# Kernel tuning notes

Measured on AMD Instinct MI355X. Metric: run time of the kernel, lower is better.

The kernel has to match this reference:

```python
import jax, jax.numpy as jnp
import numpy as np

N = 32768       # nodes
E = 65536       # directed edges
B = 512         # graphs (N // B = 64 atoms each)
DIM = 64
NUM_FEAT = 14
EDGE_DIM = 4
NET_HID = 128
CONV_STEPS = 12
S2S_STEPS = 3
NSTEM = 1024
NUM_OUT_STEM = 105

leaky = lambda v: jax.nn.leaky_relu(v, 0.01)


def setup_inputs():
    key = jax.random.key(0)
    ks = jax.random.split(key, 30)
    p = lambda i, shape, s=0.1: jax.random.normal(ks[i], shape, jnp.float32) * s
    return {
        'x': jax.random.normal(ks[0], (N, NUM_FEAT), jnp.float32),
        'edge_attr': jax.random.uniform(ks[1], (E, EDGE_DIM), jnp.float32),
        'edge_index': jax.random.randint(ks[2], (2, E), 0, N),
        'batch': jnp.arange(N, dtype=jnp.int32) // (N // B),  # sorted graph ids, all graphs non-empty
        'stem_idx': jax.random.randint(ks[3], (NSTEM,), 0, N),
        'lin0_w': p(4, (DIM, NUM_FEAT)), 'lin0_b': p(5, (DIM,)),
        'net_w1': p(6, (NET_HID, EDGE_DIM)), 'net_b1': p(7, (NET_HID,)),
        'net_w2': p(8, (DIM * DIM, NET_HID), 0.05), 'net_b2': p(9, (DIM * DIM,), 0.05),
        'conv_root': p(10, (DIM, DIM)), 'conv_bias': p(11, (DIM,)),
        'gru_w_ih': p(12, (3 * DIM, DIM)), 'gru_w_hh': p(13, (3 * DIM, DIM)),
        'gru_b_ih': p(14, (3 * DIM,)), 'gru_b_hh': p(15, (3 * DIM,)),
        'lin1_w': p(16, (8 * DIM, DIM)), 'lin1_b': p(17, (8 * DIM,)),
        'lin2_w': p(18, (NUM_OUT_STEM, 8 * DIM)), 'lin2_b': p(19, (NUM_OUT_STEM,)),
        's2s_w_ih': p(20, (4 * DIM, 2 * DIM)), 's2s_w_hh': p(21, (4 * DIM, DIM)),
        's2s_b_ih': p(22, (4 * DIM,)), 's2s_b_hh': p(23, (4 * DIM,)),
        'lin3_w': p(24, (1, 2 * DIM)), 'lin3_b': p(25, (1,)),
    }


def reference(x, edge_attr, edge_index, batch, stem_idx,
              lin0_w, lin0_b, net_w1, net_b1, net_w2, net_b2,
              conv_root, conv_bias, gru_w_ih, gru_w_hh, gru_b_ih, gru_b_hh,
              lin1_w, lin1_b, lin2_w, lin2_b,
              s2s_w_ih, s2s_w_hh, s2s_b_ih, s2s_b_hh, lin3_w, lin3_b):
    src, dst = edge_index[0], edge_index[1]

    out = leaky(x @ lin0_w.T + lin0_b)               # [N, DIM]
    h = out

    # edge-conditioned weights: constant across conv steps (edge_attr fixed), hoist
    W = (leaky(edge_attr @ net_w1.T + net_b1) @ net_w2.T + net_b2).reshape(E, DIM, DIM)

    deg = jax.ops.segment_sum(jnp.ones((E,), jnp.float32), dst, num_segments=N)
    inv_deg = (1.0 / jnp.maximum(deg, 1.0))[:, None]

    def step(carry, _):
        out, h = carry
        # NNConv: gather src feats, per-edge matmul, scatter-mean to dst, plus root term
        msg = jnp.einsum('ei,eio->eo', out[src], W)                           # [E, DIM]
        agg = jax.ops.segment_sum(msg, dst, num_segments=N) * inv_deg        # scatter-mean
        m = leaky(agg + out @ conv_root + conv_bias)
        # GRU cell (torch gate order r, z, n)
        gi = m @ gru_w_ih.T + gru_b_ih
        gh = h @ gru_w_hh.T + gru_b_hh
        ir, iz, i_n = jnp.split(gi, 3, axis=-1)
        hr, hz, hn = jnp.split(gh, 3, axis=-1)
        r = jax.nn.sigmoid(ir + hr)
        z = jax.nn.sigmoid(iz + hz)
        n = jnp.tanh(i_n + r * hn)
        h_new = (1.0 - z) * n + z * h
        return (h_new, h_new), None

    (out, h), _ = jax.lax.scan(step, (out, h), None, length=CONV_STEPS)

    # per-stem head (stem_idx = precomputed flat node indices)
    stem_feat = out[stem_idx]                                                # [NSTEM, DIM]
    per_stem_out = leaky(stem_feat @ lin1_w.T + lin1_b) @ lin2_w.T + lin2_b  # [NSTEM, 105]

    # Set2Set readout (LSTM with torch gate order i, f, g, o)
    q_star = jnp.zeros((B, 2 * DIM), jnp.float32)
    hh = jnp.zeros((B, DIM), jnp.float32)
    cc = jnp.zeros((B, DIM), jnp.float32)
    for _ in range(S2S_STEPS):
        gates = q_star @ s2s_w_ih.T + s2s_b_ih + hh @ s2s_w_hh.T + s2s_b_hh
        gi_, gf_, gg_, go_ = jnp.split(gates, 4, axis=-1)
        cc = jax.nn.sigmoid(gf_) * cc + jax.nn.sigmoid(gi_) * jnp.tanh(gg_)
        hh = jax.nn.sigmoid(go_) * jnp.tanh(cc)
        q = hh                                                               # [B, DIM]
        e = jnp.sum(out * q[batch], axis=-1)                                 # [N]
        emax = jax.ops.segment_max(e, batch, num_segments=B)
        ee = jnp.exp(e - emax[batch])
        a = ee / jax.ops.segment_sum(ee, batch, num_segments=B)[batch]       # segment softmax
        r_read = jax.ops.segment_sum(a[:, None] * out, batch, num_segments=B)
        q_star = jnp.concatenate([q, r_read], axis=-1)

    sout = q_star @ lin3_w.T + lin3_b                                        # [B, 1]
    return sout, per_stem_out


if __name__ == '__main__':
    o = reference(**setup_inputs())
    print(o[0].shape, o[1].shape)
```

## Files before the change

### kernel.cpp

```cpp
#include <hip/hip_runtime.h>
#include <hip/hip_bf16.h>

#define N_NODES   32768
#define N_EDGES   65536
#define NGRAPH    512
#define DIM       64
#define NFEAT     14
#define NHID      128
#define WCOLS     4096
#define NSTEM     1024
#define NOUT      105

typedef __attribute__((ext_vector_type(8))) short short8;
typedef __attribute__((ext_vector_type(4))) float f32x4;

__device__ __forceinline__ float bf2f(unsigned int u16) {
  union { unsigned int i; float f; } c; c.i = u16 << 16; return c.f;
}
__device__ __forceinline__ unsigned short f2bf(float f) {
  union { float f; unsigned int i; } c; c.f = f;
  return (unsigned short)((c.i + 0x7fffu + ((c.i >> 16) & 1u)) >> 16);
}
__device__ __forceinline__ float leaky(float x) { return x > 0.f ? x : 0.01f * x; }
__device__ __forceinline__ float sigm(float x) { return 1.f / (1.f + expf(-x)); }
// ... 2 lines not shown

constexpr size_t OFF_HIDP = 0;
constexpr size_t SZ_HIDP  = (size_t)N_EDGES * NHID * 2;
constexpr size_t OFF_T2T  = ALN(OFF_HIDP + SZ_HIDP);
constexpr size_t SZ_T2T   = (size_t)WCOLS * NHID * 2;
constexpr size_t OFF_B2T  = ALN(OFF_T2T + SZ_T2T);
constexpr size_t SZ_B2T   = (size_t)WCOLS * 4;
constexpr size_t OFF_STATE= ALN(OFF_B2T + SZ_B2T);
constexpr size_t SZ_STATE = (size_t)N_NODES * DIM * 4;
constexpr size_t OFF_AGG  = ALN(OFF_STATE + SZ_STATE);
constexpr size_t SZ_AGG   = SZ_STATE;
constexpr size_t OFF_IDEG = ALN(OFF_AGG + SZ_AGG);
constexpr size_t SZ_IDEG  = (size_t)N_NODES * 4;
constexpr size_t OFF_CNT  = ALN(OFF_IDEG + SZ_IDEG);
constexpr size_t SZ_CNT   = (size_t)N_NODES * 4;
constexpr size_t OFF_RP   = ALN(OFF_CNT + SZ_CNT);
constexpr size_t SZ_RP    = (size_t)(N_NODES + 1) * 4;
constexpr size_t OFF_CUR  = ALN(OFF_RP + SZ_RP);
constexpr size_t SZ_CUR   = (size_t)N_NODES * 4;
constexpr size_t OFF_SRCP = ALN(OFF_CUR + SZ_CUR);
constexpr size_t SZ_SRCP  = (size_t)N_EDGES * 4;
constexpr size_t OFF_DSTP = ALN(OFF_SRCP + SZ_SRCP);
constexpr size_t SZ_DSTP  = (size_t)N_EDGES * 4;
constexpr size_t OFF_EPOS = ALN(OFF_DSTP + SZ_DSTP);
constexpr size_t SZ_EPOS  = (size_t)N_EDGES * 4;
constexpr size_t OFF_BW1  = ALN(OFF_EPOS + SZ_EPOS);
constexpr size_t SZ_BW1   = 256 * 64 * 2;
constexpr size_t OFF_BW2  = ALN(OFF_BW1 + SZ_BW1);
constexpr size_t SZ_BW2   = 192 * 64 * 2;
constexpr size_t OFF_WIH  = ALN(OFF_BW2 + SZ_BW2);
constexpr size_t SZ_WIH   = 128 * 256 * 4;
constexpr size_t OFF_WHH  = ALN(OFF_WIH + SZ_WIH);
constexpr size_t SZ_WHH   = 64 * 256 * 4;
constexpr size_t OFF_SCL  = ALN(OFF_WHH + SZ_WHH);
constexpr size_t SZ_SCL   = (size_t)N_EDGES * 64 * 4;
constexpr size_t OFF_WT   = ALN(OFF_SCL + SZ_SCL);

__global__ void k_deg(const int* __restrict__ dst, int* __restrict__ cnt) {
  int e = blockIdx.x * 256 + threadIdx.x;
  atomicAdd(&cnt[dst[e]], 1);
}
__global__ __launch_bounds__(1024) void k_scan(const int* __restrict__ cnt,
                                               int* __restrict__ rp,
                                               int* __restrict__ cur,
                                               float* __restrict__ ideg) {
  __shared__ int part[1024];
  const int t = threadIdx.x, base = t * 32;
  int s = 0;
  for (int i = 0; i < 32; ++i) s += cnt[base + i];
  part[t] = s;
  __syncthreads();
  for (int off = 1; off < 1024; off <<= 1) {
    int v = (t >= off) ? part[t - off] : 0;
    __syncthreads();
    part[t] += v;
    __syncthreads();
  }
  int run = part[t] - s;
  for (int i = 0; i < 32; ++i) {
    int c = cnt[base + i];
    rp[base + i] = run; cur[base + i] = run;
    ideg[base + i] = 1.0f / fmaxf((float)c, 1.0f);
    run += c;
  }
  if (t == 1023) rp[N_NODES] = run;
}
__global__ void k_permute(const int* __restrict__ src, const int* __restrict__ dst,
// ... 16 lines not shown
                           const float* __restrict__ wih,
                           unsigned short* __restrict__ BW1, unsigned short* __restrict__ BW2) {
  int gid = blockIdx.x * 256 + threadIdx.x;
  if (gid >= 64 * 448) return;
  int i = gid / 448, c = gid % 448;
  if (c < 64)        BW1[c * 64 + i] = f2bf(root[i * 64 + c]);
  else if (c < 256)  BW1[c * 64 + i] = f2bf(whh[(c - 64) * 64 + i]);
  else               BW2[(c - 256) * 64 + i] = f2bf(wih[(c - 256) * 64 + i]);
}
__global__ void k_prep_s2s(const float* __restrict__ wih, const float* __restrict__ whh,
                           float* __restrict__ wihT, float* __restrict__ whhT) {
  int gid = blockIdx.x * 256 + threadIdx.x;
  if (gid < 32768) { int j = gid >> 8, k = gid & 255; wihT[gid] = wih[k * 128 + j]; }
  else { int g2 = gid - 32768; int j = g2 >> 8, k = g2 & 255; whhT[g2] = whh[k * 64 + j]; }
}
__global__ void k_lin0(const float* __restrict__ x, const float* __restrict__ w,
                       const float* __restrict__ b, float* __restrict__ state) {
  int gid = blockIdx.x * 256 + threadIdx.x;
  int n = gid >> 6, o = gid & 63;
  float acc = b[o];
  #pragma unroll
  for (int f = 0; f < NFEAT; ++f) acc += x[(size_t)n * NFEAT + f] * w[o * NFEAT + f];
  state[gid] = leaky(acc);
}
__global__ void k_hidden(const float* __restrict__ ea, const float* __restrict__ w1,
                         const float* __restrict__ b1, const int* __restrict__ epos,
                         unsigned short* __restrict__ hid_p) {
  int gid = blockIdx.x * 256 + threadIdx.x;
  int e = gid >> 7, h = gid & 127;
  float acc = b1[h];
  #pragma unroll
  for (int d = 0; d < 4; ++d) acc += ea[(size_t)e * 4 + d] * w1[h * 4 + d];
  hid_p[(size_t)epos[e] * 128 + h] = f2bf(leaky(acc));
}

#define WG_PAD 136
__global__ __launch_bounds__(256) void k_wgemm(const unsigned short* __restrict__ A,
                                               const unsigned short* __restrict__ Bt,
                                               const float* __restrict__ b2t,
                                               unsigned char* __restrict__ W8,
                                               float* __restrict__ SCL) {
  __shared__ __align__(16) unsigned short As[64 * WG_PAD];
  __shared__ __align__(16) unsigned short Bs[64 * WG_PAD];
  __shared__ __align__(16) char pk[64][64];
  const int nb = blockIdx.x, mb = blockIdx.y, t = threadIdx.x;
  #pragma unroll
  for (int j = 0; j < 4; ++j) {
    int c = t + 256 * j;
    int row = c >> 4, col8 = (c & 15) * 8;
    *reinterpret_cast<uint4*>(&As[row * WG_PAD + col8]) =
        *reinterpret_cast<const uint4*>(A + (size_t)(mb * 64 + row) * 128 + col8);
    *reinterpret_cast<uint4*>(&Bs[row * WG_PAD + col8]) =
        *reinterpret_cast<const uint4*>(Bt + (size_t)(nb * 64 + row) * 128 + col8);
  }
  __syncthreads();
  const int wv = t >> 6, ln = t & 63, r = ln & 15, g = ln >> 4;
  f32x4 acc[4] = {};
  #pragma unroll
  for (int ks = 0; ks < 4; ++ks) {
    int k0 = ks * 32 + g * 8;
    short8 a = *reinterpret_cast<const short8*>(&As[(wv * 16 + r) * WG_PAD + k0]);
    #pragma unroll
    for (int nt = 0; nt < 4; ++nt) {
      short8 b = *reinterpret_cast<const short8*>(&Bs[(nt * 16 + r) * WG_PAD + k0]);
      acc[nt] = __builtin_amdgcn_mfma_f32_16x16x32_bf16(a, b, acc[nt], 0, 0, 0);
    }
  }
  float bias[4];
  #pragma unroll
  for (int nt = 0; nt < 4; ++nt) bias[nt] = b2t[nb * 64 + nt * 16 + r];
  #pragma unroll
  for (int j = 0; j < 4; ++j) {
    int e_l = wv * 16 + g * 4 + j;
    float w[4], m = 0.f;
    #pragma unroll
    for (int nt = 0; nt < 4; ++nt) { w[nt] = acc[nt][j] + bias[nt]; m = fmaxf(m, fabsf(w[nt])); }
    m = fmaxf(m, __shfl_xor(m, 1)); m = fmaxf(m, __shfl_xor(m, 2));
    m = fmaxf(m, __shfl_xor(m, 4)); m = fmaxf(m, __shfl_xor(m, 8));
    float inv = m > 0.f ? 127.f / m : 0.f;
    #pragma unroll
    for (int nt = 0; nt < 4; ++nt)
      pk[e_l][nt * 16 + r] = (char)(int)rintf(w[nt] * inv);
    if (r == 0) {
      size_t e8 = (size_t)mb * 64 + e_l;
      SCL[e8 * 64 + nb] = m * (1.f / 127.f);
    }
  }
  __syncthreads();
  {
    int e_l = t >> 2, jc = t & 3;
    size_t e8 = (size_t)mb * 64 + e_l;
    *reinterpret_cast<uint4*>(W8 + e8 * 4096 + jc * 1024 + nb * 16) =
        *reinterpret_cast<const uint4*>(&pk[e_l][jc * 16]);
  }
}

__global__ __launch_bounds__(256) void k_msg_csr(const unsigned char* __restrict__ W8,
                                                 const float* __restrict__ SCL,
                                                 int lim8,
                                                 const int* __restrict__ rp,
                                                 const int* __restrict__ src_p,
                                                 const float* __restrict__ state,
                                                 const float* __restrict__ ideg,
                                                 float* __restrict__ agg) {
  const int wv = threadIdx.x >> 6, ln = threadIdx.x & 63;
  const int d = blockIdx.x * 4 + wv;
  const int k0 = rp[d], k1 = rp[d + 1];
  float acc = 0.f;
  for (int k = k0; k < k1; ++k) {
    if (k >= lim8) continue;
    const int src = src_p[k];
    const float sval = state[(size_t)src * 64 + ln];
    const unsigned char* wp = W8 + (size_t)k * 4096 + ln * 16;
    float sub = 0.f;
    #pragma unroll
    for (int j = 0; j < 4; ++j) {
      uint4 v = *reinterpret_cast<const uint4*>(wp + j * 1024);
      unsigned int u[4] = {v.x, v.y, v.z, v.w};
      #pragma unroll
      for (int q = 0; q < 4; ++q) {
        int i0 = j * 16 + q * 4;
        sub = fmaf((float)(int)(char)(u[q] & 0xff),         __shfl(sval, i0),     sub);
        sub = fmaf((float)(int)(char)((u[q] >> 8) & 0xff),  __shfl(sval, i0 + 1), sub);
        sub = fmaf((float)(int)(char)((u[q] >> 16) & 0xff), __shfl(sval, i0 + 2), sub);
        sub = fmaf((float)(int)(char)(u[q] >> 24),          __shfl(sval, i0 + 3), sub);
      }
    }
    acc = fmaf(sub, SCL[(size_t)k * 64 + ln], acc);
  }
  agg[(size_t)d * 64 + ln] = acc * ideg[d];
}

#define WM_PAD 136
__global__ __launch_bounds__(256) void k_wmsg(const unsigned short* __restrict__ hid,
                                              const unsigned short* __restrict__ T2t,
                                              const float* __restrict__ b2t,
                                              const float* __restrict__ state,
                                              const int* __restrict__ srcs,
                                              const int* __restrict__ dsts,
                                              const float* __restrict__ ideg,
                                              int e0,
                                              float* __restrict__ agg) {
  __shared__ __align__(16) unsigned short As[64 * WM_PAD];
  __shared__ __align__(16) unsigned short Bs[2][64 * WM_PAD];
  __shared__ __align__(16) float Ss[64][68];
  __shared__ int dstl[64]; __shared__ float idgl[64];
  __shared__ int srcl[64];
  const int t = threadIdx.x;
  const int eb = blockIdx.x * 64;
  if (t < 64) {
    int e = e0 + eb + t;
    srcl[t] = srcs[e];
    int d = dsts[e]; dstl[t] = d; idgl[t] = ideg[d];
  }
  __syncthreads();
  #pragma unroll
  for (int j = 0; j < 4; ++j) {
    int c = t + 256 * j;
    int row = c >> 4, col8 = (c & 15) * 8;
    *reinterpret_cast<uint4*>(&As[row * WM_PAD + col8]) =
        *reinterpret_cast<const uint4*>(hid + (size_t)(eb + row) * 128 + col8);
  }
  #pragma unroll
  for (int j = 0; j < 4; ++j) {
    int c = t + 256 * j;
    int row = c >> 4, q = (c & 15) * 4;
    *reinterpret_cast<float4*>(&Ss[row][q]) =
        *reinterpret_cast<const float4*>(state + (size_t)srcl[row] * 64 + q);
  }
  #pragma unroll
  for (int j = 0; j < 4; ++j) {
    int c = t + 256 * j;
    int row = c >> 4, col8 = (c & 15) * 8;
    *reinterpret_cast<uint4*>(&Bs[0][row * WM_PAD + col8]) =
        *reinterpret_cast<const uint4*>(T2t + (size_t)row * 128 + col8);
  }
  __syncthreads();
  const int wv = t >> 6, ln = t & 63, r = ln & 15, g = ln >> 4;
  for (int nb = 0; nb < 64; ++nb) {
    const int cur = nb & 1;
    if (nb + 1 < 64) {
      #pragma unroll
      for (int j = 0; j < 4; ++j) {
        int c = t + 256 * j;
        int row = c >> 4, col8 = (c & 15) * 8;
        *reinterpret_cast<uint4*>(&Bs[cur ^ 1][row * WM_PAD + col8]) =
            *reinterpret_cast<const uint4*>(T2t + (size_t)((nb + 1) * 64 + row) * 128 + col8);
      }
    }
    f32x4 acc[4] = {};
    #pragma unroll
    for (int ks = 0; ks < 4; ++ks) {
      int k0 = ks * 32 + g * 8;
      short8 a = *reinterpret_cast<const short8*>(&As[(wv * 16 + r) * WM_PAD + k0]);
      #pragma unroll
      for (int nt = 0; nt < 4; ++nt) {
        short8 b = *reinterpret_cast<const short8*>(&Bs[cur][(nt * 16 + r) * WM_PAD + k0]);
        acc[nt] = __builtin_amdgcn_mfma_f32_16x16x32_bf16(a, b, acc[nt], 0, 0, 0);
      }
    }
    float bias[4];
    #pragma unroll
    for (int nt = 0; nt < 4; ++nt) bias[nt] = b2t[nb * 64 + nt * 16 + r];
    float pj[4];
    #pragma unroll
    for (int j = 0; j < 4; ++j) {
      int row = wv * 16 + g * 4 + j;
      float p = 0.f;
      #pragma unroll
      for (int nt = 0; nt < 4; ++nt)
        p += (acc[nt][j] + bias[nt]) * Ss[row][nt * 16 + r];
      pj[j] = p;
    }
    #pragma unroll
    for (int j = 0; j < 4; ++j) {
      float p = pj[j];
      p += __shfl_xor(p, 1); p += __shfl_xor(p, 2);
      p += __shfl_xor(p, 4); p += __shfl_xor(p, 8);
      pj[j] = p;
    }
    if (r == 0) {
      #pragma unroll
      for (int j = 0; j < 4; ++j) {
        int row = wv * 16 + g * 4 + j;
        atomicAdd(&agg[(size_t)dstl[row] * 64 + nb], pj[j] * idgl[row]);
      }
    }
    __syncthreads();
  }
}

#define KPAD 72
__global__ __launch_bounds__(512, 1) void k_gru(const float* __restrict__ agg,
                                                float* __restrict__ state,
                                                const unsigned short* __restrict__ BW1,
                                                const unsigned short* __restrict__ BW2,
                                                const float* __restrict__ conv_bias,
                                                const float* __restrict__ b_ih,
                                                const float* __restrict__ b_hh) {
  __shared__ __align__(16) unsigned short As[128 * KPAD];
  __shared__ __align__(16) unsigned short Ms[128 * KPAD];
  __shared__ __align__(16) unsigned short B1s[256 * KPAD];
  __shared__ __align__(16) unsigned short B2s[192 * KPAD];
  const int t = threadIdx.x;
  const int rowbase = blockIdx.x * 128;
  #pragma unroll
  for (int j = 0; j < 2; ++j) {
    int c = t + 512 * j;
    int row = c >> 3, col8 = (c & 7) * 8;
    const float* sp = state + (size_t)(rowbase + row) * 64 + col8;
    float4 f0 = *reinterpret_cast<const float4*>(sp);
    float4 f1 = *reinterpret_cast<const float4*>(sp + 4);
    short8 hv;
    hv[0] = (short)f2bf(f0.x); hv[1] = (short)f2bf(f0.y);
    hv[2] = (short)f2bf(f0.z); hv[3] = (short)f2bf(f0.w);
    hv[4] = (short)f2bf(f1.x); hv[5] = (short)f2bf(f1.y);
    hv[6] = (short)f2bf(f1.z); hv[7] = (short)f2bf(f1.w);
    *reinterpret_cast<short8*>(&As[row * KPAD + col8]) = hv;
  }
  #pragma unroll
  for (int j = 0; j < 4; ++j) {
    int c = t + 512 * j;
    int row = c >> 3, col8 = (c & 7) * 8;
    *reinterpret_cast<uint4*>(&B1s[row * KPAD + col8]) =
        *reinterpret_cast<const uint4*>(BW1 + row * 64 + col8);
  }
  #pragma unroll
  for (int j = 0; j < 3; ++j) {
    int c = t + 512 * j;
    int row = c >> 3, col8 = (c & 7) * 8;
    *reinterpret_cast<uint4*>(&B2s[row * KPAD + col8]) =
        *reinterpret_cast<const uint4*>(BW2 + row * 64 + col8);
  }
  __syncthreads();
  const int wv = t >> 6, ln = t & 63, r = ln & 15, g = ln >> 4;
  f32x4 acc1[16] = {};
  #pragma unroll
  for (int ks = 0; ks < 2; ++ks) {
    int k0 = ks * 32 + g * 8;
    short8 a = *reinterpret_cast<const short8*>(&As[(wv * 16 + r) * KPAD + k0]);
    #pragma unroll
    for (int nt = 0; nt < 16; ++nt) {
      short8 b = *reinterpret_cast<const short8*>(&B1s[(nt * 16 + r) * KPAD + k0]);
      acc1[nt] = __builtin_amdgcn_mfma_f32_16x16x32_bf16(a, b, acc1[nt], 0, 0, 0);
    }
  }
  #pragma unroll
  for (int nt = 0; nt < 4; ++nt) {
    int col = nt * 16 + r;
    float cb = conv_bias[col];
    #pragma unroll
    for (int j = 0; j < 4; ++j) {
      int lrow = wv * 16 + g * 4 + j;
      float mv = agg[(size_t)(rowbase + lrow) * 64 + col] + acc1[nt][j] + cb;
      Ms[lrow * KPAD + col] = f2bf(leaky(mv));
    }
  }
  __syncthreads();
  f32x4 acc2[12] = {};
  #pragma unroll
  for (int ks = 0; ks < 2; ++ks) {
    int k0 = ks * 32 + g * 8;
    short8 a = *reinterpret_cast<const short8*>(&Ms[(wv * 16 + r) * KPAD + k0]);
    #pragma unroll
    for (int nt = 0; nt < 12; ++nt) {
      short8 b = *reinterpret_cast<const short8*>(&B2s[(nt * 16 + r) * KPAD + k0]);
      acc2[nt] = __builtin_amdgcn_mfma_f32_16x16x32_bf16(a, b, acc2[nt], 0, 0, 0);
    }
  }
  #pragma unroll
  for (int nt = 0; nt < 4; ++nt) {
    int o = nt * 16 + r;
    float bir = b_ih[o],       bhr = b_hh[o];
    float biz = b_ih[64 + o],  bhz = b_hh[64 + o];
    float bin = b_ih[128 + o], bhn = b_hh[128 + o];
    #pragma unroll
    for (int j = 0; j < 4; ++j) {
      size_t gidx = (size_t)(rowbase + wv * 16 + g * 4 + j) * 64 + o;
      float rr = sigm(acc2[nt][j] + bir + acc1[4 + nt][j] + bhr);
      float zz = sigm(acc2[4 + nt][j] + biz + acc1[8 + nt][j] + bhz);
      float nn = tanhf(acc2[8 + nt][j] + bin + rr * (acc1[12 + nt][j] + bhn));
      float hold = state[gidx];
      state[gidx] = (1.f - zz) * nn + zz * hold;
    }
  }
}

__global__ __launch_bounds__(256) void k_s2s(const float* __restrict__ state,
                                             const float* __restrict__ wihT,
                                             const float* __restrict__ whhT,
                                             const float* __restrict__ b_ih,
                                             const float* __restrict__ b_hh,
                                             const float* __restrict__ lin3_w,
                                             const float* __restrict__ lin3_b,
                                             float* __restrict__ d_out) {
  __shared__ float tile[64 * 65];
  __shared__ float qs[128], hhs[64], ccs[64], gates[256], attw[64];
  const int g = blockIdx.x, t = threadIdx.x;
  for (int c = t; c < 64 * 64; c += 256) {
    int row = c >> 6, col = c & 63;
    tile[row * 65 + col] = state[(size_t)(g * 64 + row) * 64 + col];
  }
  if (t < 128) qs[t] = 0.f;
  if (t < 64) { hhs[t] = 0.f; ccs[t] = 0.f; }
  __syncthreads();
  for (int it = 0; it < 3; ++it) {
    float acc = b_ih[t] + b_hh[t];
    for (int j = 0; j < 128; ++j) acc += qs[j] * wihT[j * 256 + t];
    for (int j = 0; j < 64; ++j)  acc += hhs[j] * whhT[j * 256 + t];
    gates[t] = acc;
    __syncthreads();
    if (t < 64) {
      float ci = sigm(gates[t]), cf = sigm(gates[64 + t]);
      float cg = tanhf(gates[128 + t]), co = sigm(gates[192 + t]);
      float c2 = cf * ccs[t] + ci * cg;
      ccs[t] = c2;
      float h2 = co * tanhf(c2);
// ... 30 lines not shown
                                              const float* __restrict__ w1,
                                              const float* __restrict__ b1,
                                              const float* __restrict__ w2,
                                              const float* __restrict__ b2,
                                              float* __restrict__ d_out) {
  __shared__ float feat[64];
  __shared__ float hidl[512];
  const int t = threadIdx.x, s = blockIdx.x;
  if (t < 64) feat[t] = state[(size_t)stem_idx[s] * 64 + t];
  __syncthreads();
  {
    const float* wr = w1 + (size_t)t * 64;
    float a0 = 0.f, a1 = 0.f, a2 = 0.f, a3 = 0.f;
    #pragma unroll
    for (int i = 0; i < 64; i += 16) {
      float4 x0 = *reinterpret_cast<const float4*>(wr + i);
      float4 x1 = *reinterpret_cast<const float4*>(wr + i + 4);
      float4 x2 = *reinterpret_cast<const float4*>(wr + i + 8);
      float4 x3 = *reinterpret_cast<const float4*>(wr + i + 12);
      a0 += x0.x*feat[i]    + x0.y*feat[i+1]  + x0.z*feat[i+2]  + x0.w*feat[i+3];
      a1 += x1.x*feat[i+4]  + x1.y*feat[i+5]  + x1.z*feat[i+6]  + x1.w*feat[i+7];
      a2 += x2.x*feat[i+8]  + x2.y*feat[i+9]  + x2.z*feat[i+10] + x2.w*feat[i+11];
      a3 += x3.x*feat[i+12] + x3.y*feat[i+13] + x3.z*feat[i+14] + x3.w*feat[i+15];
    }
    hidl[t] = leaky(a0 + a1 + a2 + a3 + b1[t]);
  }
  __syncthreads();
  if (t < 4 * NOUT) {
    int o = t >> 2, q = t & 3;
    const float* wr = w2 + (size_t)o * 512 + q * 128;
    const float* hr = hidl + q * 128;
    float a0 = 0.f, a1 = 0.f, a2 = 0.f, a3 = 0.f;
    #pragma unroll
    for (int k = 0; k < 128; k += 16) {
      float4 x0 = *reinterpret_cast<const float4*>(wr + k);
      float4 x1 = *reinterpret_cast<const float4*>(wr + k + 4);
      float4 x2 = *reinterpret_cast<const float4*>(wr + k + 8);
      float4 x3 = *reinterpret_cast<const float4*>(wr + k + 12);
      a0 += x0.x*hr[k]    + x0.y*hr[k+1]  + x0.z*hr[k+2]  + x0.w*hr[k+3];
      a1 += x1.x*hr[k+4]  + x1.y*hr[k+5]  + x1.z*hr[k+6]  + x1.w*hr[k+7];
      a2 += x2.x*hr[k+8]  + x2.y*hr[k+9]  + x2.z*hr[k+10] + x2.w*hr[k+11];
      a3 += x3.x*hr[k+12] + x3.y*hr[k+13] + x3.z*hr[k+14] + x3.w*hr[k+15];
    }
    float p = a0 + a1 + a2 + a3;
    p += __shfl_xor(p, 1); p += __shfl_xor(p, 2);
    if (q == 0) d_out[512 + (size_t)s * NOUT + o] = p + b2[o];
  }
}

extern "C" void kernel_launch(void* const* d_in, const int* in_sizes, int n_in,
                              void* d_out, int out_size, void* d_ws, size_t ws_size,
                              hipStream_t stream) {
  (void)in_sizes; (void)n_in; (void)out_size;
  if (ws_size < OFF_WT) return;

  long pe8 = (long)((ws_size - OFF_WT) / 4096);
  if (pe8 > N_EDGES) pe8 = N_EDGES;
  pe8 &= ~63L;
  const int LIM8 = (int)pe8;
  const int TE = N_EDGES - LIM8;

  const float* x         = (const float*)d_in[0];
  const float* edge_attr = (const float*)d_in[1];
  const int*   eidx      = (const int*)d_in[2];
  const int*   stem_idx  = (const int*)d_in[4];
  const float* lin0_w = (const float*)d_in[5];
  const float* lin0_b = (const float*)d_in[6];
  const float* net_w1 = (const float*)d_in[7];
  const float* net_b1 = (const float*)d_in[8];
  const float* net_w2 = (const float*)d_in[9];
  const float* net_b2 = (const float*)d_in[10];
  const float* conv_root = (const float*)d_in[11];
  const float* conv_bias = (const float*)d_in[12];
  const float* gru_w_ih = (const float*)d_in[13];
  const float* gru_w_hh = (const float*)d_in[14];
  const float* gru_b_ih = (const float*)d_in[15];
  const float* gru_b_hh = (const float*)d_in[16];
  const float* lin1_w = (const float*)d_in[17];
  const float* lin1_b = (const float*)d_in[18];
  const float* lin2_w = (const float*)d_in[19];
  const float* lin2_b = (const float*)d_in[20];
  const float* s2s_w_ih = (const float*)d_in[21];
  const float* s2s_w_hh = (const float*)d_in[22];
  const float* s2s_b_ih = (const float*)d_in[23];
  const float* s2s_b_hh = (const float*)d_in[24];
  const float* lin3_w = (const float*)d_in[25];
  const float* lin3_b = (const float*)d_in[26];

  char* ws = (char*)d_ws;
  unsigned short* hid_p = (unsigned short*)(ws + OFF_HIDP);
  unsigned short* T2t  = (unsigned short*)(ws + OFF_T2T);
  float*          b2t  = (float*)(ws + OFF_B2T);
  float*          state= (float*)(ws + OFF_STATE);
  float*          agg  = (float*)(ws + OFF_AGG);
  float*          ideg = (float*)(ws + OFF_IDEG);
  int*            cnt  = (int*)(ws + OFF_CNT);
  int*            rp   = (int*)(ws + OFF_RP);
  int*            cur  = (int*)(ws + OFF_CUR);
  int*            src_p= (int*)(ws + OFF_SRCP);
  int*            dst_p= (int*)(ws + OFF_DSTP);
  int*            epos = (int*)(ws + OFF_EPOS);
  unsigned short* BW1  = (unsigned short*)(ws + OFF_BW1);
  unsigned short* BW2  = (unsigned short*)(ws + OFF_BW2);
  float*          wihT = (float*)(ws + OFF_WIH);
  float*          whhT = (float*)(ws + OFF_WHH);
  float*          SCL  = (float*)(ws + OFF_SCL);
  unsigned char*  W8   = (unsigned char*)(ws + OFF_WT);
  float* out = (float*)d_out;

  const int* src = eidx;
  const int* dst = eidx + N_EDGES;

  hipMemsetAsync(cnt, 0, SZ_CNT, stream);
  k_deg<<<N_EDGES / 256, 256, 0, stream>>>(dst, cnt);
  k_scan<<<1, 1024, 0, stream>>>(cnt, rp, cur, ideg);
  k_permute<<<N_EDGES / 256, 256, 0, stream>>>(src, dst, cur, src_p, dst_p, epos);
  k_prep_t2<<<(WCOLS * NHID) / 256, 256, 0, stream>>>(net_w2, net_b2, T2t, b2t);
  k_prep_gru<<<112, 256, 0, stream>>>(conv_root, gru_w_hh, gru_w_ih, BW1, BW2);
  k_prep_s2s<<<192, 256, 0, stream>>>(s2s_w_ih, s2s_w_hh, wihT, whhT);
  k_lin0<<<(N_NODES * DIM) / 256, 256, 0, stream>>>(x, lin0_w, lin0_b, state);
  k_hidden<<<(N_EDGES * NHID) / 256, 256, 0, stream>>>(edge_attr, net_w1, net_b1,
                                                       epos, hid_p);
  if (LIM8 > 0)
    k_wgemm<<<dim3(WCOLS / 64, LIM8 / 64), 256, 0, stream>>>(hid_p, T2t, b2t, W8, SCL);

  for (int s = 0; s < 12; ++s) {
    k_msg_csr<<<N_NODES / 4, 256, 0, stream>>>(W8, SCL, LIM8, rp, src_p,
                                               state, ideg, agg);
    if (TE > 0)
      k_wmsg<<<(TE + 63) / 64, 256, 0, stream>>>(hid_p + (size_t)LIM8 * NHID, T2t, b2t,
                                                 state, src_p, dst_p, ideg, LIM8, agg);
    k_gru<<<N_NODES / 128, 512, 0, stream>>>(agg, state, BW1, BW2, conv_bias,
                                             gru_b_ih, gru_b_hh);
  }

  k_s2s<<<NGRAPH, 256, 0, stream>>>(state, wihT, whhT, s2s_b_ih, s2s_b_hh,
                                    lin3_w, lin3_b, out);
  k_stem<<<NSTEM, 512, 0, stream>>>(state, stem_idx, lin1_w, lin1_b,
                                    lin2_w, lin2_b, out);
}
```

Before: 2.090 ms.

## Reuse A tile across column blocks in wgemm and unroll int8 message loop

k_wgemm now keeps the A tile in shared memory and loops over 8 column blocks per workgroup, double-buffering the B tiles and writing scales in one vectorized store at the end. This cuts redundant A loads and the launch grid. k_msg_csr processes two edges per iteration, reads the source row directly from global/cache with a scalar-broadcast index instead of wave shuffles, and clamps the loop bound rather than branching per edge. The LIM8 rounding changes to a multiple of 512, which may push a few more edges onto the slower on-the-fly path when workspace is limited.

```diff
diff --git a/kernel.cpp b/kernel.cpp
--- a/kernel.cpp
+++ b/kernel.cpp
@@ -150,58 +150,87 @@
                                                unsigned char* __restrict__ W8,
                                                float* __restrict__ SCL) {
   __shared__ __align__(16) unsigned short As[64 * WG_PAD];
-  __shared__ __align__(16) unsigned short Bs[64 * WG_PAD];
+  __shared__ __align__(16) unsigned short Bs[2][64 * WG_PAD];
   __shared__ __align__(16) char pk[64][64];
-  const int nb = blockIdx.x, mb = blockIdx.y, t = threadIdx.x;
+  __shared__ float sclAll[64][8];
+  const int nb0 = blockIdx.x * 8, mb = blockIdx.y, t = threadIdx.x;
   #pragma unroll
   for (int j = 0; j < 4; ++j) {
     int c = t + 256 * j;
     int row = c >> 4, col8 = (c & 15) * 8;
     *reinterpret_cast<uint4*>(&As[row * WG_PAD + col8]) =
         *reinterpret_cast<const uint4*>(A + (size_t)(mb * 64 + row) * 128 + col8);
-    *reinterpret_cast<uint4*>(&Bs[row * WG_PAD + col8]) =
-        *reinterpret_cast<const uint4*>(Bt + (size_t)(nb * 64 + row) * 128 + col8);
+    *reinterpret_cast<uint4*>(&Bs[0][row * WG_PAD + col8]) =
+        *reinterpret_cast<const uint4*>(Bt + (size_t)(nb0 * 64 + row) * 128 + col8);
   }
   __syncthreads();
   const int wv = t >> 6, ln = t & 63, r = ln & 15, g = ln >> 4;
-  f32x4 acc[4] = {};
-  #pragma unroll
-  for (int ks = 0; ks < 4; ++ks) {
-    int k0 = ks * 32 + g * 8;
-    short8 a = *reinterpret_cast<const short8*>(&As[(wv * 16 + r) * WG_PAD + k0]);
-    #pragma unroll
-    for (int nt = 0; nt < 4; ++nt) {
-      short8 b = *reinterpret_cast<const short8*>(&Bs[(nt * 16 + r) * WG_PAD + k0]);
-      acc[nt] = __builtin_amdgcn_mfma_f32_16x16x32_bf16(a, b, acc[nt], 0, 0, 0);
-    }
-  }
-  float bias[4];
-  #pragma unroll
-  for (int nt = 0; nt < 4; ++nt) bias[nt] = b2t[nb * 64 + nt * 16 + r];
-  #pragma unroll
-  for (int j = 0; j < 4; ++j) {
-    int e_l = wv * 16 + g * 4 + j;
-    float w[4], m = 0.f;
-    #pragma unroll
-    for (int nt = 0; nt < 4; ++nt) { w[nt] = acc[nt][j] + bias[nt]; m = fmaxf(m, fabsf(w[nt])); }
-    m = fmaxf(m, __shfl_xor(m, 1)); m = fmaxf(m, __shfl_xor(m, 2));
-    m = fmaxf(m, __shfl_xor(m, 4)); m = fmaxf(m, __shfl_xor(m, 8));
-    float inv = m > 0.f ? 127.f / m : 0.f;
-    #pragma unroll
-    for (int nt = 0; nt < 4; ++nt)
-      pk[e_l][nt * 16 + r] = (char)(int)rintf(w[nt] * inv);
-    if (r == 0) {
-      size_t e8 = (size_t)mb * 64 + e_l;
-      SCL[e8 * 64 + nb] = m * (1.f / 127.f);
-    }
-  }
-  __syncthreads();
-  {
-    int e_l = t >> 2, jc = t & 3;
-    size_t e8 = (size_t)mb * 64 + e_l;
-    *reinterpret_cast<uint4*>(W8 + e8 * 4096 + jc * 1024 + nb * 16) =
-        *reinterpret_cast<const uint4*>(&pk[e_l][jc * 16]);
-  }
+  for (int nbi = 0; nbi < 8; ++nbi) {
+    const int cur = nbi & 1;
+    const int nb = nb0 + nbi;
+    if (nbi + 1 < 8) {
+      #pragma unroll
+      for (int j = 0; j < 4; ++j) {
+        int c = t + 256 * j;
+        int row = c >> 4, col8 = (c & 15) * 8;
+        *reinterpret_cast<uint4*>(&Bs[cur ^ 1][row * WG_PAD + col8]) =
+            *reinterpret_cast<const uint4*>(Bt + (size_t)((nb + 1) * 64 + row) * 128 + col8);
+      }
+    }
+    f32x4 acc[4] = {};
+    #pragma unroll
+    for (int ks = 0; ks < 4; ++ks) {
+      int kk = ks * 32 + g * 8;
+      short8 a = *reinterpret_cast<const short8*>(&As[(wv * 16 + r) * WG_PAD + kk]);
+      #pragma unroll
+      for (int nt = 0; nt < 4; ++nt) {
+        short8 b = *reinterpret_cast<const short8*>(&Bs[cur][(nt * 16 + r) * WG_PAD + kk]);
+        acc[nt] = __builtin_amdgcn_mfma_f32_16x16x32_bf16(a, b, acc[nt], 0, 0, 0);
+      }
+    }
+    float bias[4];
+    #pragma unroll
+    for (int nt = 0; nt < 4; ++nt) bias[nt] = b2t[nb * 64 + nt * 16 + r];
+    #pragma unroll
+    for (int j = 0; j < 4; ++j) {
+      int e_l = wv * 16 + g * 4 + j;
+      float w[4], m = 0.f;
+      #pragma unroll
+      for (int nt = 0; nt < 4; ++nt) { w[nt] = acc[nt][j] + bias[nt]; m = fmaxf(m, fabsf(w[nt])); }
+      m = fmaxf(m, __shfl_xor(m, 1)); m = fmaxf(m, __shfl_xor(m, 2));
+      m = fmaxf(m, __shfl_xor(m, 4)); m = fmaxf(m, __shfl_xor(m, 8));
+      float inv = m > 0.f ? 127.f / m : 0.f;
+      #pragma unroll
+      for (int nt = 0; nt < 4; ++nt)
+        pk[e_l][nt * 16 + r] = (char)(int)rintf(w[nt] * inv);
+      if (r == 0) sclAll[e_l][nbi] = m * (1.f / 127.f);
+    }
+    __syncthreads();
+    {
+      int e_l = t >> 2, jc = t & 3;
+      *reinterpret_cast<uint4*>(W8 + ((size_t)(mb * 64) + e_l) * 4096 + jc * 1024 + nb * 16) =
+          *reinterpret_cast<const uint4*>(&pk[e_l][jc * 16]);
+    }
+    __syncthreads();
+  }
+  if (t < 64) {
+    float* sp = SCL + ((size_t)(mb * 64) + t) * 64 + nb0;
+    *reinterpret_cast<float4*>(sp)     = *reinterpret_cast<const float4*>(&sclAll[t][0]);
+    *reinterpret_cast<float4*>(sp + 4) = *reinterpret_cast<const float4*>(&sclAll[t][4]);
+  }
+}
+
+__device__ __forceinline__ float dot16(uint4 v, const float* __restrict__ s) {
+  unsigned int u[4] = {v.x, v.y, v.z, v.w};
+  float p0 = 0.f, p1 = 0.f;
+  #pragma unroll
+  for (int q = 0; q < 4; ++q) {
+    p0 = fmaf((float)(int)(char)(u[q] & 0xff),         s[q * 4 + 0], p0);
+    p1 = fmaf((float)(int)(char)((u[q] >> 8) & 0xff),  s[q * 4 + 1], p1);
+    p0 = fmaf((float)(int)(char)((u[q] >> 16) & 0xff), s[q * 4 + 2], p0);
+    p1 = fmaf((float)(int)(char)(u[q] >> 24),          s[q * 4 + 3], p1);
+  }
+  return p0 + p1;
 }
 
 __global__ __launch_bounds__(256) void k_msg_csr(const unsigned char* __restrict__ W8,
@@ -214,28 +243,42 @@
                                                  float* __restrict__ agg) {
   const int wv = threadIdx.x >> 6, ln = threadIdx.x & 63;
   const int d = blockIdx.x * 4 + wv;
-  const int k0 = rp[d], k1 = rp[d + 1];
+  int k0 = rp[d], k1 = rp[d + 1];
+  if (k1 > lim8) k1 = lim8;
   float acc = 0.f;
-  for (int k = k0; k < k1; ++k) {
-    if (k >= lim8) continue;
-    const int src = src_p[k];
-    const float sval = state[(size_t)src * 64 + ln];
-    const unsigned char* wp = W8 + (size_t)k * 4096 + ln * 16;
-    float sub = 0.f;
-    #pragma unroll
-    for (int j = 0; j < 4; ++j) {
-      uint4 v = *reinterpret_cast<const uint4*>(wp + j * 1024);
-      unsigned int u[4] = {v.x, v.y, v.z, v.w};
-      #pragma unroll
-      for (int q = 0; q < 4; ++q) {
-        int i0 = j * 16 + q * 4;
-        sub = fmaf((float)(int)(char)(u[q] & 0xff),         __shfl(sval, i0),     sub);
-        sub = fmaf((float)(int)(char)((u[q] >> 8) & 0xff),  __shfl(sval, i0 + 1), sub);
-        sub = fmaf((float)(int)(char)((u[q] >> 16) & 0xff), __shfl(sval, i0 + 2), sub);
-        sub = fmaf((float)(int)(char)(u[q] >> 24),          __shfl(sval, i0 + 3), sub);
-      }
-    }
-    acc = fmaf(sub, SCL[(size_t)k * 64 + ln], acc);
+  int k = k0;
+  for (; k + 2 <= k1; k += 2) {
+    const unsigned char* w0 = W8 + (size_t)k * 4096 + ln * 16;
+    uint4 a0 = *reinterpret_cast<const uint4*>(w0);
+    uint4 a1 = *reinterpret_cast<const uint4*>(w0 + 1024);
+    uint4 a2 = *reinterpret_cast<const uint4*>(w0 + 2048);
+    uint4 a3 = *reinterpret_cast<const uint4*>(w0 + 3072);
+    uint4 b0 = *reinterpret_cast<const uint4*>(w0 + 4096);
+    uint4 b1 = *reinterpret_cast<const uint4*>(w0 + 5120);
+    uint4 b2 = *reinterpret_cast<const uint4*>(w0 + 6144);
+    uint4 b3 = *reinterpret_cast<const uint4*>(w0 + 7168);
+    float sA = SCL[(size_t)k * 64 + ln];
+    float sB = SCL[(size_t)k * 64 + 64 + ln];
+    int s0 = __builtin_amdgcn_readfirstlane(src_p[k]);
+    int s1 = __builtin_amdgcn_readfirstlane(src_p[k + 1]);
+    const float* r0 = state + (size_t)s0 * 64;
+    const float* r1 = state + (size_t)s1 * 64;
+    float dA = (dot16(a0, r0) + dot16(a1, r0 + 16)) + (dot16(a2, r0 + 32) + dot16(a3, r0 + 48));
+    float dB = (dot16(b0, r1) + dot16(b1, r1 + 16)) + (dot16(b2, r1 + 32) + dot16(b3, r1 + 48));
+    acc = fmaf(dA, sA, acc);
+    acc = fmaf(dB, sB, acc);
+  }
+  if (k < k1) {
+    const unsigned char* w0 = W8 + (size_t)k * 4096 + ln * 16;
+    uint4 a0 = *reinterpret_cast<const uint4*>(w0);
+    uint4 a1 = *reinterpret_cast<const uint4*>(w0 + 1024);
+    uint4 a2 = *reinterpret_cast<const uint4*>(w0 + 2048);
+    uint4 a3 = *reinterpret_cast<const uint4*>(w0 + 3072);
+    float sA = SCL[(size_t)k * 64 + ln];
+    int s0 = __builtin_amdgcn_readfirstlane(src_p[k]);
+    const float* r0 = state + (size_t)s0 * 64;
+    float dA = (dot16(a0, r0) + dot16(a1, r0 + 16)) + (dot16(a2, r0 + 32) + dot16(a3, r0 + 48));
+    acc = fmaf(dA, sA, acc);
   }
   agg[(size_t)d * 64 + ln] = acc * ideg[d];
 }
@@ -300,11 +343,11 @@
     f32x4 acc[4] = {};
     #pragma unroll
     for (int ks = 0; ks < 4; ++ks) {
-      int k0 = ks * 32 + g * 8;
-      short8 a = *reinterpret_cast<const short8*>(&As[(wv * 16 + r) * WM_PAD + k0]);
+      int kk = ks * 32 + g * 8;
+      short8 a = *reinterpret_cast<const short8*>(&As[(wv * 16 + r) * WM_PAD + kk]);
       #pragma unroll
       for (int nt = 0; nt < 4; ++nt) {
-        short8 b = *reinterpret_cast<const short8*>(&Bs[cur][(nt * 16 + r) * WM_PAD + k0]);
+        short8 b = *reinterpret_cast<const short8*>(&Bs[cur][(nt * 16 + r) * WM_PAD + kk]);
         acc[nt] = __builtin_amdgcn_mfma_f32_16x16x32_bf16(a, b, acc[nt], 0, 0, 0);
       }
     }
@@ -386,11 +429,11 @@
   f32x4 acc1[16] = {};
   #pragma unroll
   for (int ks = 0; ks < 2; ++ks) {
-    int k0 = ks * 32 + g * 8;
-    short8 a = *reinterpret_cast<const short8*>(&As[(wv * 16 + r) * KPAD + k0]);
+    int kk = ks * 32 + g * 8;
+    short8 a = *reinterpret_cast<const short8*>(&As[(wv * 16 + r) * KPAD + kk]);
     #pragma unroll
     for (int nt = 0; nt < 16; ++nt) {
-      short8 b = *reinterpret_cast<const short8*>(&B1s[(nt * 16 + r) * KPAD + k0]);
+      short8 b = *reinterpret_cast<const short8*>(&B1s[(nt * 16 + r) * KPAD + kk]);
       acc1[nt] = __builtin_amdgcn_mfma_f32_16x16x32_bf16(a, b, acc1[nt], 0, 0, 0);
     }
   }
@@ -409,11 +452,11 @@
   f32x4 acc2[12] = {};
   #pragma unroll
   for (int ks = 0; ks < 2; ++ks) {
-    int k0 = ks * 32 + g * 8;
-    short8 a = *reinterpret_cast<const short8*>(&Ms[(wv * 16 + r) * KPAD + k0]);
+    int kk = ks * 32 + g * 8;
+    short8 a = *reinterpret_cast<const short8*>(&Ms[(wv * 16 + r) * KPAD + kk]);
     #pragma unroll
     for (int nt = 0; nt < 12; ++nt) {
-      short8 b = *reinterpret_cast<const short8*>(&B2s[(nt * 16 + r) * KPAD + k0]);
+      short8 b = *reinterpret_cast<const short8*>(&B2s[(nt * 16 + r) * KPAD + kk]);
       acc2[nt] = __builtin_amdgcn_mfma_f32_16x16x32_bf16(a, b, acc2[nt], 0, 0, 0);
     }
   }
@@ -528,15 +571,15 @@
     const float* hr = hidl + q * 128;
     float a0 = 0.f, a1 = 0.f, a2 = 0.f, a3 = 0.f;
     #pragma unroll
-    for (int k = 0; k < 128; k += 16) {
-      float4 x0 = *reinterpret_cast<const float4*>(wr + k);
-      float4 x1 = *reinterpret_cast<const float4*>(wr + k + 4);
-      float4 x2 = *reinterpret_cast<const float4*>(wr + k + 8);
-      float4 x3 = *reinterpret_cast<const float4*>(wr + k + 12);
-      a0 += x0.x*hr[k]    + x0.y*hr[k+1]  + x0.z*hr[k+2]  + x0.w*hr[k+3];
-      a1 += x1.x*hr[k+4]  + x1.y*hr[k+5]  + x1.z*hr[k+6]  + x1.w*hr[k+7];
-      a2 += x2.x*hr[k+8]  + x2.y*hr[k+9]  + x2.z*hr[k+10] + x2.w*hr[k+11];
-      a3 += x3.x*hr[k+12] + x3.y*hr[k+13] + x3.z*hr[k+14] + x3.w*hr[k+15];
+    for (int kk = 0; kk < 128; kk += 16) {
+      float4 x0 = *reinterpret_cast<const float4*>(wr + kk);
+      float4 x1 = *reinterpret_cast<const float4*>(wr + kk + 4);
+      float4 x2 = *reinterpret_cast<const float4*>(wr + kk + 8);
+      float4 x3 = *reinterpret_cast<const float4*>(wr + kk + 12);
+      a0 += x0.x*hr[kk]    + x0.y*hr[kk+1]  + x0.z*hr[kk+2]  + x0.w*hr[kk+3];
+      a1 += x1.x*hr[kk+4]  + x1.y*hr[kk+5]  + x1.z*hr[kk+6]  + x1.w*hr[kk+7];
+      a2 += x2.x*hr[kk+8]  + x2.y*hr[kk+9]  + x2.z*hr[kk+10] + x2.w*hr[kk+11];
+      a3 += x3.x*hr[kk+12] + x3.y*hr[kk+13] + x3.z*hr[kk+14] + x3.w*hr[kk+15];
     }
     float p = a0 + a1 + a2 + a3;
     p += __shfl_xor(p, 1); p += __shfl_xor(p, 2);
@@ -552,7 +595,7 @@
 
   long pe8 = (long)((ws_size - OFF_WT) / 4096);
   if (pe8 > N_EDGES) pe8 = N_EDGES;
-  pe8 &= ~63L;
+  pe8 &= ~511L;
   const int LIM8 = (int)pe8;
   const int TE = N_EDGES - LIM8;
 
@@ -618,7 +661,7 @@
   k_hidden<<<(N_EDGES * NHID) / 256, 256, 0, stream>>>(edge_attr, net_w1, net_b1,
                                                        epos, hid_p);
   if (LIM8 > 0)
-    k_wgemm<<<dim3(WCOLS / 64, LIM8 / 64), 256, 0, stream>>>(hid_p, T2t, b2t, W8, SCL);
+    k_wgemm<<<dim3(8, LIM8 / 64), 256, 0, stream>>>(hid_p, T2t, b2t, W8, SCL);
 
   for (int s = 0; s < 12; ++s) {
     k_msg_csr<<<N_NODES / 4, 256, 0, stream>>>(W8, SCL, LIM8, rp, src_p,
```

New measurement: 2.069 ms. No clear change (-1.0%).

## Quantize node state to int8 and use sdot4 for edge messages

Applied to the files above, without the earlier changes.

Node state is quantized to int8 with a per-node scale, once after lin0 and then inside the GRU epilogue each step. The message kernel then computes the per-edge 64x64 matvec with packed int8 dot4 instructions instead of unpacking bytes and broadcasting floats with shuffles. It also processes two edges per iteration and takes the source index through readfirstlane. The aim is to cut the ALU and shuffle cost of the message pass, at the price of extra quantization error in the state and some added work in the GRU epilogue.

```diff
diff --git a/kernel.cpp b/kernel.cpp
--- a/kernel.cpp
+++ b/kernel.cpp
@@ -58,7 +58,11 @@
 constexpr size_t SZ_WIH   = 128 * 256 * 4;
 constexpr size_t OFF_WHH  = ALN(OFF_WIH + SZ_WIH);
 constexpr size_t SZ_WHH   = 64 * 256 * 4;
-constexpr size_t OFF_SCL  = ALN(OFF_WHH + SZ_WHH);
+constexpr size_t OFF_S8   = ALN(OFF_WHH + SZ_WHH);
+constexpr size_t SZ_S8    = (size_t)N_NODES * 64;
+constexpr size_t OFF_SSC  = ALN(OFF_S8 + SZ_S8);
+constexpr size_t SZ_SSC   = (size_t)N_NODES * 4;
+constexpr size_t OFF_SCL  = ALN(OFF_SSC + SZ_SSC);
 constexpr size_t SZ_SCL   = (size_t)N_EDGES * 64 * 4;
 constexpr size_t OFF_WT   = ALN(OFF_SCL + SZ_SCL);
 
@@ -141,6 +145,28 @@
   #pragma unroll
   for (int d = 0; d < 4; ++d) acc += ea[(size_t)e * 4 + d] * w1[h * 4 + d];
   hid_p[(size_t)epos[e] * 128 + h] = f2bf(leaky(acc));
+}
+__global__ __launch_bounds__(256) void k_qstate(const float* __restrict__ state,
+                                                char* __restrict__ s8,
+                                                float* __restrict__ sscale) {
+  __shared__ char q8[4][64];
+  __shared__ float scs[4];
+  const int t = threadIdx.x, wv = t >> 6, ln = t & 63;
+  const int n = blockIdx.x * 4 + wv;
+  float v = state[(size_t)n * 64 + ln];
+  float m = fabsf(v);
+  #pragma unroll
+  for (int off = 1; off < 64; off <<= 1) m = fmaxf(m, __shfl_xor(m, off));
+  float inv = m > 0.f ? 127.f / m : 0.f;
+  q8[wv][ln] = (char)(int)rintf(v * inv);
+  if (ln == 0) scs[wv] = m * (1.f / 127.f);
+  __syncthreads();
+  if (t < 64) {
+    int w2 = t >> 4, c = t & 15;
+    reinterpret_cast<int*>(s8)[((size_t)(blockIdx.x * 4 + w2)) * 16 + c] =
+        reinterpret_cast<const int*>(q8[w2])[c];
+  }
+  if (t < 4) sscale[blockIdx.x * 4 + t] = scs[t];
 }
 
 #define WG_PAD 136
@@ -167,11 +193,11 @@
   f32x4 acc[4] = {};
   #pragma unroll
   for (int ks = 0; ks < 4; ++ks) {
-    int k0 = ks * 32 + g * 8;
-    short8 a = *reinterpret_cast<const short8*>(&As[(wv * 16 + r) * WG_PAD + k0]);
+    int kk = ks * 32 + g * 8;
+    short8 a = *reinterpret_cast<const short8*>(&As[(wv * 16 + r) * WG_PAD + kk]);
     #pragma unroll
     for (int nt = 0; nt < 4; ++nt) {
-      short8 b = *reinterpret_cast<const short8*>(&Bs[(nt * 16 + r) * WG_PAD + k0]);
+      short8 b = *reinterpret_cast<const short8*>(&Bs[(nt * 16 + r) * WG_PAD + kk]);
       acc[nt] = __builtin_amdgcn_mfma_f32_16x16x32_bf16(a, b, acc[nt], 0, 0, 0);
     }
   }
@@ -204,38 +230,54 @@
   }
 }
 
+__device__ __forceinline__ int dot64(const uint4* __restrict__ wp, const int* __restrict__ s) {
+  int u = 0;
+  #pragma unroll
+  for (int j = 0; j < 4; ++j) {
+    uint4 v = wp[j * 64];
+    u = __builtin_amdgcn_sdot4((int)v.x, s[j * 4 + 0], u, false);
+    u = __builtin_amdgcn_sdot4((int)v.y, s[j * 4 + 1], u, false);
+    u = __builtin_amdgcn_sdot4((int)v.z, s[j * 4 + 2], u, false);
+    u = __builtin_amdgcn_sdot4((int)v.w, s[j * 4 + 3], u, false);
+  }
+  return u;
+}
+
 __global__ __launch_bounds__(256) void k_msg_csr(const unsigned char* __restrict__ W8,
                                                  const float* __restrict__ SCL,
+                                                 const char* __restrict__ s8,
+                                                 const float* __restrict__ sscale,
                                                  int lim8,
                                                  const int* __restrict__ rp,
                                                  const int* __restrict__ src_p,
-                                                 const float* __restrict__ state,
                                                  const float* __restrict__ ideg,
                                                  float* __restrict__ agg) {
   const int wv = threadIdx.x >> 6, ln = threadIdx.x & 63;
   const int d = blockIdx.x * 4 + wv;
-  const int k0 = rp[d], k1 = rp[d + 1];
+  int k0 = rp[d], k1 = rp[d + 1];
+  if (k1 > lim8) k1 = lim8;
   float acc = 0.f;
-  for (int k = k0; k < k1; ++k) {
-    if (k >= lim8) continue;
-    const int src = src_p[k];
-    const float sval = state[(size_t)src * 64 + ln];
-    const unsigned char* wp = W8 + (size_t)k * 4096 + ln * 16;
-    float sub = 0.f;
-    #pragma unroll
-    for (int j = 0; j < 4; ++j) {
-      uint4 v = *reinterpret_cast<const uint4*>(wp + j * 1024);
-      unsigned int u[4] = {v.x, v.y, v.z, v.w};
-      #pragma unroll
-      for (int q = 0; q < 4; ++q) {
-        int i0 = j * 16 + q * 4;
-        sub = fmaf((float)(int)(char)(u[q] & 0xff),         __shfl(sval, i0),     sub);
-        sub = fmaf((float)(int)(char)((u[q] >> 8) & 0xff),  __shfl(sval, i0 + 1), sub);
-        sub = fmaf((float)(int)(char)((u[q] >> 16) & 0xff), __shfl(sval, i0 + 2), sub);
-        sub = fmaf((float)(int)(char)(u[q] >> 24),          __shfl(sval, i0 + 3), sub);
-      }
-    }
-    acc = fmaf(sub, SCL[(size_t)k * 64 + ln], acc);
+  int k = k0;
+  for (; k + 2 <= k1; k += 2) {
+    const uint4* wA = reinterpret_cast<const uint4*>(W8 + (size_t)k * 4096 + ln * 16);
+    const uint4* wB = reinterpret_cast<const uint4*>(W8 + (size_t)(k + 1) * 4096 + ln * 16);
+    int sA = __builtin_amdgcn_readfirstlane(src_p[k]);
+    int sB = __builtin_amdgcn_readfirstlane(src_p[k + 1]);
+    const int* rA = reinterpret_cast<const int*>(s8 + (size_t)sA * 64);
+    const int* rB = reinterpret_cast<const int*>(s8 + (size_t)sB * 64);
+    float fA = SCL[(size_t)k * 64 + ln] * sscale[sA];
+    float fB = SCL[(size_t)k * 64 + 64 + ln] * sscale[sB];
+    int uA = dot64(wA, rA);
+    int uB = dot64(wB, rB);
+    acc = fmaf((float)uA, fA, acc);
+    acc = fmaf((float)uB, fB, acc);
+  }
+  if (k < k1) {
+    const uint4* wA = reinterpret_cast<const uint4*>(W8 + (size_t)k * 4096 + ln * 16);
+    int sA = __builtin_amdgcn_readfirstlane(src_p[k]);
+    const int* rA = reinterpret_cast<const int*>(s8 + (size_t)sA * 64);
+    float fA = SCL[(size_t)k * 64 + ln] * sscale[sA];
+    acc = fmaf((float)dot64(wA, rA), fA, acc);
   }
   agg[(size_t)d * 64 + ln] = acc * ideg[d];
 }
@@ -300,11 +342,11 @@
     f32x4 acc[4] = {};
     #pragma unroll
     for (int ks = 0; ks < 4; ++ks) {
-      int k0 = ks * 32 + g * 8;
-      short8 a = *reinterpret_cast<const short8*>(&As[(wv * 16 + r) * WM_PAD + k0]);
+      int kk = ks * 32 + g * 8;
+      short8 a = *reinterpret_cast<const short8*>(&As[(wv * 16 + r) * WM_PAD + kk]);
       #pragma unroll
       for (int nt = 0; nt < 4; ++nt) {
-        short8 b = *reinterpret_cast<const short8*>(&Bs[cur][(nt * 16 + r) * WM_PAD + k0]);
+        short8 b = *reinterpret_cast<const short8*>(&Bs[cur][(nt * 16 + r) * WM_PAD + kk]);
         acc[nt] = __builtin_amdgcn_mfma_f32_16x16x32_bf16(a, b, acc[nt], 0, 0, 0);
       }
     }
@@ -346,7 +388,9 @@
                                                 const unsigned short* __restrict__ BW2,
                                                 const float* __restrict__ conv_bias,
                                                 const float* __restrict__ b_ih,
-                                                const float* __restrict__ b_hh) {
+                                                const float* __restrict__ b_hh,
+                                                char* __restrict__ s8,
+                                                float* __restrict__ sscale) {
   __shared__ __align__(16) unsigned short As[128 * KPAD];
   __shared__ __align__(16) unsigned short Ms[128 * KPAD];
   __shared__ __align__(16) unsigned short B1s[256 * KPAD];
@@ -386,11 +430,11 @@
   f32x4 acc1[16] = {};
   #pragma unroll
   for (int ks = 0; ks < 2; ++ks) {
-    int k0 = ks * 32 + g * 8;
-    short8 a = *reinterpret_cast<const short8*>(&As[(wv * 16 + r) * KPAD + k0]);
+    int kk = ks * 32 + g * 8;
+    short8 a = *reinterpret_cast<const short8*>(&As[(wv * 16 + r) * KPAD + kk]);
     #pragma unroll
     for (int nt = 0; nt < 16; ++nt) {
-      short8 b = *reinterpret_cast<const short8*>(&B1s[(nt * 16 + r) * KPAD + k0]);
+      short8 b = *reinterpret_cast<const short8*>(&B1s[(nt * 16 + r) * KPAD + kk]);
       acc1[nt] = __builtin_amdgcn_mfma_f32_16x16x32_bf16(a, b, acc1[nt], 0, 0, 0);
     }
   }
@@ -409,14 +453,15 @@
   f32x4 acc2[12] = {};
   #pragma unroll
   for (int ks = 0; ks < 2; ++ks) {
-    int k0 = ks * 32 + g * 8;
-    short8 a = *reinterpret_cast<const short8*>(&Ms[(wv * 16 + r) * KPAD + k0]);
+    int kk = ks * 32 + g * 8;
+    short8 a = *reinterpret_cast<const short8*>(&Ms[(wv * 16 + r) * KPAD + kk]);
     #pragma unroll
     for (int nt = 0; nt < 12; ++nt) {
-      short8 b = *reinterpret_cast<const short8*>(&B2s[(nt * 16 + r) * KPAD + k0]);
+      short8 b = *reinterpret_cast<const short8*>(&B2s[(nt * 16 + r) * KPAD + kk]);
       acc2[nt] = __builtin_amdgcn_mfma_f32_16x16x32_bf16(a, b, acc2[nt], 0, 0, 0);
     }
   }
+  float hnew[4][4];
   #pragma unroll
   for (int nt = 0; nt < 4; ++nt) {
     int o = nt * 16 + r;
@@ -430,8 +475,31 @@
       float zz = sigm(acc2[4 + nt][j] + biz + acc1[8 + nt][j] + bhz);
       float nn = tanhf(acc2[8 + nt][j] + bin + rr * (acc1[12 + nt][j] + bhn));
       float hold = state[gidx];
-      state[gidx] = (1.f - zz) * nn + zz * hold;
-    }
+      float hv = (1.f - zz) * nn + zz * hold;
+      state[gidx] = hv;
+      hnew[nt][j] = hv;
+    }
+  }
+  char* s8t = (char*)As;
+  #pragma unroll
+  for (int j = 0; j < 4; ++j) {
+    float mx = 0.f;
+    #pragma unroll
+    for (int nt = 0; nt < 4; ++nt) mx = fmaxf(mx, fabsf(hnew[nt][j]));
+    mx = fmaxf(mx, __shfl_xor(mx, 1)); mx = fmaxf(mx, __shfl_xor(mx, 2));
+    mx = fmaxf(mx, __shfl_xor(mx, 4)); mx = fmaxf(mx, __shfl_xor(mx, 8));
+    float inv = mx > 0.f ? 127.f / mx : 0.f;
+    int lrow = wv * 16 + g * 4 + j;
+    #pragma unroll
+    for (int nt = 0; nt < 4; ++nt)
+      s8t[lrow * 64 + nt * 16 + r] = (char)(int)rintf(hnew[nt][j] * inv);
+    if (r == 0) sscale[rowbase + lrow] = mx * (1.f / 127.f);
+  }
+  __syncthreads();
+  {
+    int row = t >> 2, c = t & 3;
+    *reinterpret_cast<uint4*>(s8 + ((size_t)(rowbase + row)) * 64 + c * 16) =
+        *reinterpret_cast<const uint4*>(s8t + row * 64 + c * 16);
   }
 }
 
@@ -528,15 +596,15 @@
     const float* hr = hidl + q * 128;
     float a0 = 0.f, a1 = 0.f, a2 = 0.f, a3 = 0.f;
     #pragma unroll
-    for (int k = 0; k < 128; k += 16) {
-      float4 x0 = *reinterpret_cast<const float4*>(wr + k);
-      float4 x1 = *reinterpret_cast<const float4*>(wr + k + 4);
-      float4 x2 = *reinterpret_cast<const float4*>(wr + k + 8);
-      float4 x3 = *reinterpret_cast<const float4*>(wr + k + 12);
-      a0 += x0.x*hr[k]    + x0.y*hr[k+1]  + x0.z*hr[k+2]  + x0.w*hr[k+3];
-      a1 += x1.x*hr[k+4]  + x1.y*hr[k+5]  + x1.z*hr[k+6]  + x1.w*hr[k+7];
-      a2 += x2.x*hr[k+8]  + x2.y*hr[k+9]  + x2.z*hr[k+10] + x2.w*hr[k+11];
-      a3 += x3.x*hr[k+12] + x3.y*hr[k+13] + x3.z*hr[k+14] + x3.w*hr[k+15];
+    for (int kk = 0; kk < 128; kk += 16) {
+      float4 x0 = *reinterpret_cast<const float4*>(wr + kk);
+      float4 x1 = *reinterpret_cast<const float4*>(wr + kk + 4);
+      float4 x2 = *reinterpret_cast<const float4*>(wr + kk + 8);
+      float4 x3 = *reinterpret_cast<const float4*>(wr + kk + 12);
+      a0 += x0.x*hr[kk]    + x0.y*hr[kk+1]  + x0.z*hr[kk+2]  + x0.w*hr[kk+3];
+      a1 += x1.x*hr[kk+4]  + x1.y*hr[kk+5]  + x1.z*hr[kk+6]  + x1.w*hr[kk+7];
+      a2 += x2.x*hr[kk+8]  + x2.y*hr[kk+9]  + x2.z*hr[kk+10] + x2.w*hr[kk+11];
+      a3 += x3.x*hr[kk+12] + x3.y*hr[kk+13] + x3.z*hr[kk+14] + x3.w*hr[kk+15];
     }
     float p = a0 + a1 + a2 + a3;
     p += __shfl_xor(p, 1); p += __shfl_xor(p, 2);
@@ -600,6 +668,8 @@
   unsigned short* BW2  = (unsigned short*)(ws + OFF_BW2);
   float*          wihT = (float*)(ws + OFF_WIH);
   float*          whhT = (float*)(ws + OFF_WHH);
+  char*           s8   = (char*)(ws + OFF_S8);
+  float*          sscale = (float*)(ws + OFF_SSC);
   float*          SCL  = (float*)(ws + OFF_SCL);
   unsigned char*  W8   = (unsigned char*)(ws + OFF_WT);
   float* out = (float*)d_out;
@@ -615,19 +685,20 @@
   k_prep_gru<<<112, 256, 0, stream>>>(conv_root, gru_w_hh, gru_w_ih, BW1, BW2);
   k_prep_s2s<<<192, 256, 0, stream>>>(s2s_w_ih, s2s_w_hh, wihT, whhT);
   k_lin0<<<(N_NODES * DIM) / 256, 256, 0, stream>>>(x, lin0_w, lin0_b, state);
+  k_qstate<<<N_NODES / 4, 256, 0, stream>>>(state, s8, sscale);
   k_hidden<<<(N_EDGES * NHID) / 256, 256, 0, stream>>>(edge_attr, net_w1, net_b1,
                                                        epos, hid_p);
   if (LIM8 > 0)
     k_wgemm<<<dim3(WCOLS / 64, LIM8 / 64), 256, 0, stream>>>(hid_p, T2t, b2t, W8, SCL);
 
   for (int s = 0; s < 12; ++s) {
-    k_msg_csr<<<N_NODES / 4, 256, 0, stream>>>(W8, SCL, LIM8, rp, src_p,
-                                               state, ideg, agg);
+    k_msg_csr<<<N_NODES / 4, 256, 0, stream>>>(W8, SCL, s8, sscale, LIM8,
+                                               rp, src_p, ideg, agg);
     if (TE > 0)
       k_wmsg<<<(TE + 63) / 64, 256, 0, stream>>>(hid_p + (size_t)LIM8 * NHID, T2t, b2t,
                                                  state, src_p, dst_p, ideg, LIM8, agg);
     k_gru<<<N_NODES / 128, 512, 0, stream>>>(agg, state, BW1, BW2, conv_bias,
-                                             gru_b_ih, gru_b_hh);
+                                             gru_b_ih, gru_b_hh, s8, sscale);
   }
 
   k_s2s<<<NGRAPH, 256, 0, stream>>>(state, wihT, whhT, s2s_b_ih, s2s_b_hh,
```

Measured after the change: 1.981 ms. -5.2%, faster.
